# Kernel optimization log

Hardware: AMD Instinct MI355X
Metric: run time of the kernel (lower is better)

## Reference

```python
import jax, jax.numpy as jnp
import numpy as np

D_MODEL = 512
NUM_HEADS = 8
D_K = D_MODEL // NUM_HEADS


def setup_inputs() -> dict:
    key = jax.random.key(0)
    ks = jax.random.split(key, 12)
    B, Sq, Sk = 4, 2048, 2048
    scale = 1.0 / np.sqrt(D_MODEL)
    inp = {
        'query': jax.random.normal(ks[0], (B, Sq, D_MODEL), jnp.float32),
        'key':   jax.random.normal(ks[1], (B, Sk, D_MODEL), jnp.float32),
        'value': jax.random.normal(ks[2], (B, Sk, D_MODEL), jnp.float32),
        'wq': jax.random.normal(ks[3], (D_MODEL, D_MODEL), jnp.float32) * scale,
        'bq': jnp.zeros((D_MODEL,), jnp.float32),
        'wk': jax.random.normal(ks[4], (D_MODEL, D_MODEL), jnp.float32) * scale,
        'bk': jnp.zeros((D_MODEL,), jnp.float32),
        'wv': jax.random.normal(ks[5], (D_MODEL, D_MODEL), jnp.float32) * scale,
        'bv': jnp.zeros((D_MODEL,), jnp.float32),
        'wo': jax.random.normal(ks[6], (D_MODEL, D_MODEL), jnp.float32) * scale,
        'bo': jnp.zeros((D_MODEL,), jnp.float32),
        'ln_g': jnp.ones((D_MODEL,), jnp.float32),
        'ln_b': jnp.zeros((D_MODEL,), jnp.float32),
    }
    return inp


def _layer_norm(x, g, b, eps=1e-5):
    mu = jnp.mean(x, axis=-1, keepdims=True)
    var = jnp.mean(jnp.square(x - mu), axis=-1, keepdims=True)
    return (x - mu) * jax.lax.rsqrt(var + eps) * g + b


def reference(query, key, value, wq, bq, wk, bk, wv, bv, wo, bo, ln_g, ln_b):
    B, Sq, _ = query.shape
    Sk = key.shape[1]
    residual = query
    # projections: torch Linear computes x @ W^T + b; here wq is (out,in)-free:
    # we store weights as (d_model, d_model) and use x @ W + b (equivalent param space)
    Q = (query @ wq + bq).reshape(B, Sq, NUM_HEADS, D_K).transpose(0, 2, 1, 3)
    K = (key   @ wk + bk).reshape(B, Sk, NUM_HEADS, D_K).transpose(0, 2, 1, 3)
    V = (value @ wv + bv).reshape(B, Sk, NUM_HEADS, D_K).transpose(0, 2, 1, 3)
    scores = jnp.einsum('bhqd,bhkd->bhqk', Q, K) / jnp.sqrt(jnp.float32(D_K))
    attn = jax.nn.softmax(scores, axis=-1)  # dropout is identity in eval
    context = jnp.einsum('bhqk,bhkd->bhqd', attn, V)
    context = context.transpose(0, 2, 1, 3).reshape(B, Sq, D_MODEL)
    out = context @ wo + bo
    return _layer_norm(out + residual, ln_g, ln_b)
```

## Files before the change

### kernel.cpp

```cpp
#include <hip/hip_runtime.h>
#include <cstdint>
#include <cstddef>

typedef unsigned short u16;
typedef __bf16 bf16x8 __attribute__((ext_vector_type(8)));
typedef __bf16 bf16x4 __attribute__((ext_vector_type(4)));
typedef float f32x4 __attribute__((ext_vector_type(4)));

#define DEVI __device__ __forceinline__

DEVI u16 f2bf(float f){
  union { float f; unsigned u; } v; v.f = f;
  unsigned r = v.u + 0x7fffu + ((v.u >> 16) & 1u);
  return (u16)(r >> 16);
}

#if defined(__has_builtin)
#if __has_builtin(__builtin_amdgcn_exp2f)
#define EXP2F(x) __builtin_amdgcn_exp2f(x)
#else
#define EXP2F(x) exp2f(x)
#endif
#else
#define EXP2F(x) exp2f(x)
#endif

#define MFMA16(a,b,c) __builtin_amdgcn_mfma_f32_16x16x32_bf16((a),(b),(c),0,0,0)

DEVI void gload_lds16(const void* g, void* l){
  __builtin_amdgcn_global_load_lds(
      (const __attribute__((address_space(1))) void*)g,
      (__attribute__((address_space(3))) void*)l, 16, 0, 0);
}

#define PIPE_SYNC do{ asm volatile("s_waitcnt vmcnt(0)" ::: "memory"); \
    __builtin_amdgcn_s_barrier(); \
    __builtin_amdgcn_sched_barrier(0); }while(0)


__global__ void k_prep_x(const float* __restrict__ q, const float* __restrict__ k,
                         const float* __restrict__ v, u16* __restrict__ xb){
  size_t t = (size_t)blockIdx.x*blockDim.x + threadIdx.x;
  size_t base = t*8;
  const float* s;
  if (base < 4194304u)      s = q + base;
  else if (base < 8388608u) s = k + (base - 4194304u);
  else                      s = v + (base - 8388608u);
  float4 a = *(const float4*)s;
  float4 b = *(const float4*)(s+4);
  ushort4 o0, o1;
  o0.x=f2bf(a.x); o0.y=f2bf(a.y); o0.z=f2bf(a.z); o0.w=f2bf(a.w);
  o1.x=f2bf(b.x); o1.y=f2bf(b.y); o1.z=f2bf(b.z); o1.w=f2bf(b.w);
  *(ushort4*)(xb + base)     = o0;
  *(ushort4*)(xb + base + 4) = o1;
}

__global__ void k_prep_w(const float* __restrict__ w0, const float* __restrict__ w1,
                         const float* __restrict__ w2, const float* __restrict__ w3,
                         u16* __restrict__ wt){
  __shared__ u16 tile[64][72];
  int p = blockIdx.z;
  const float* W = (p==0)?w0:((p==1)?w1:((p==2)?w2:w3));
  int k0 = blockIdx.x*64, n0 = blockIdx.y*64;
  int t = threadIdx.x;
  int tr = t >> 4, tc = t & 15;
  #pragma unroll
  for (int pass=0; pass<4; pass++){
    int row = pass*16 + tr;
    float4 a = *(const float4*)(W + (size_t)(k0+row)*512 + n0 + tc*4);
    tile[row][tc*4+0] = f2bf(a.x);
    tile[row][tc*4+1] = f2bf(a.y);
    tile[row][tc*4+2] = f2bf(a.z);
    tile[row][tc*4+3] = f2bf(a.w);
  }
  __syncthreads();
  #pragma unroll
  for (int pass=0; pass<4; pass++){
    int n = pass*16 + tr;
    ushort4 o;
    o.x = tile[tc*4+0][n];
    o.y = tile[tc*4+1][n];
    o.z = tile[tc*4+2][n];
    o.w = tile[tc*4+3][n];
    *(ushort4*)(wt + (size_t)p*262144 + (size_t)(n0+n)*512 + k0 + tc*4) = o;
  }
}

__global__ __launch_bounds__(256)
void k_gemm_qkv(const u16* __restrict__ xb, const u16* __restrict__ wt,
                const float* __restrict__ bq, const float* __restrict__ bk,
                const float* __restrict__ bv,
                u16* __restrict__ qb, u16* __restrict__ kb, u16* __restrict__ vt){
  int l = threadIdx.x & 63, w = threadIdx.x >> 6;
  int lr = l & 15, lg = l >> 4;
  int f = blockIdx.x;
  int xcd = f & 7, j0 = f >> 3;
  int pm   = xcd*24 + (j0 >> 2);
  int nblk = j0 & 3;
  int p    = pm >> 6, mblk = pm & 63;
  int wr = w >> 1, wc = w & 1;

  const float* bias = (p==0)?bq:((p==1)?bk:bv);
  float osc = (p==0)? (0.125f*1.44269504088896340736f) : 1.0f;

  const char* Ag = (const char*)(xb + (size_t)p*4194304 + (size_t)mblk*128*512);
  const char* Bg = (const char*)(wt + (size_t)p*262144  + (size_t)nblk*128*512);

  __shared__ __align__(16) u16 Albuf[2][8192];
  __shared__ __align__(16) u16 Blbuf[2][8192];

  int r8 = l >> 3, sl = l & 7;

  #define STAGE_G(t, buf) do{ \
    _Pragma("unroll") \
    for (int cc=0; cc<4; ++cc){ \
      int c = w*4 + cc; int row = c*8 + r8; \
      int sw = (sl ^ (row & 7)) << 4; \
      gload_lds16(Ag + (size_t)row*1024 + (size_t)(t)*128 + sw, (char*)Albuf[buf] + c*1024); \
      gload_lds16(Bg + (size_t)row*1024 + (size_t)(t)*128 + sw, (char*)Blbuf[buf] + c*1024); \
    } }while(0)

  STAGE_G(0, 0);
  PIPE_SYNC;

  f32x4 acc[4][4] = {};
  for (int t = 0; t < 8; ++t){
    int cur = t & 1;
    if (t < 7) STAGE_G(t+1, cur^1);
    const char* Ac = (const char*)Albuf[cur];
    const char* Bc = (const char*)Blbuf[cur];
    #pragma unroll
    for (int kk=0;kk<2;kk++){
      int ks = ((kk*4 + lg) ^ (lr & 7)) << 4;
      bf16x8 af[4], bfr[4];
      #pragma unroll
      for (int i=0;i<4;i++)
        af[i]  = *(const bf16x8*)(Ac + (wr*64 + i*16 + lr)*128 + ks);
      #pragma unroll
      for (int j=0;j<4;j++)
        bfr[j] = *(const bf16x8*)(Bc + (wc*64 + j*16 + lr)*128 + ks);
      #pragma unroll
      for (int i=0;i<4;i++)
        #pragma unroll
        for (int j=0;j<4;j++)
          acc[i][j] = MFMA16(af[i], bfr[j], acc[i][j]);
    }
    if (t < 7) PIPE_SYNC;
  }
  #undef STAGE_G

  int m0 = mblk*128 + wr*64;
  int n0 = nblk*128 + wc*64;
  if (p < 2){
    u16* outp = (p==0)?qb:kb;
    #pragma unroll
    for (int i=0;i<4;i++){
      #pragma unroll
      for (int j=0;j<4;j++){
        int n = n0 + j*16 + lr;
        int h = n >> 6, d = n & 63;
        float bb = bias[n];
        #pragma unroll
        for (int rg=0;rg<4;rg++){
          int m = m0 + i*16 + 4*lg + rg;
          int b = m >> 11, s = m & 2047;
          float val = (acc[i][j][rg] + bb)*osc;
          __bf16 hb = (__bf16)val;
          outp[(((size_t)b*8 + h)*2048 + s)*64 + d] = *(u16*)&hb;
        }
      }
    }
  } else {
    #pragma unroll
    for (int i=0;i<4;i++){
      #pragma unroll
      for (int j=0;j<4;j++){
        int n = n0 + j*16 + lr;
        int h = n >> 6, d = n & 63;
        float bb = bias[n];
        int m = m0 + i*16 + 4*lg;
        int b = m >> 11, s = m & 2047;
        ushort4 o;
        #pragma unroll
        for (int rg=0;rg<4;rg++){
          __bf16 hb = (__bf16)(acc[i][j][rg] + bb);
          ((u16*)&o)[rg] = *(u16*)&hb;
        }
        *(ushort4*)(vt + (((size_t)(b*8+h)*64 + d)*2048 + s)) = o;
      }
    }
  }
}

__global__ __launch_bounds__(512, 4)
void k_attn(const u16* __restrict__ qbuf, const u16* __restrict__ kbuf,
            const u16* __restrict__ vtb, u16* __restrict__ opart,
            float* __restrict__ lpart){
  int l = threadIdx.x & 63, w = threadIdx.x >> 6;
  int lr = l & 15, lg = l >> 4;
  int f = blockIdx.x;
  int bh    = (f & 7)*4 + ((f >> 3) & 3);
  int rest  = f >> 5;
  int split = rest & 1;
  int q0    = (rest >> 1)*256 + w*32;
  int b = bh >> 3, h = bh & 7;
  int kvbase = split*1024;

  const u16* Qp = qbuf + ((size_t)bh*2048 + q0)*64;
  const char* Kg = (const char*)(kbuf + (size_t)bh*2048*64) + (size_t)kvbase*128;
  const char* Vg = (const char*)(vtb  + (size_t)bh*64*2048) + (size_t)kvbase*2;

  __shared__ __align__(16) u16 Klds[2][4096];
  __shared__ __align__(16) u16 Vlds[2][4096];
  __shared__ __align__(16) u16 Plds[8][2048];
  u16* Pw = Plds[w];

  int r8 = l >> 3, sl = l & 7;

  bf16x8 qf[2][2];
  #pragma unroll
  for (int j=0;j<2;j++)
    #pragma unroll
    for (int kk=0;kk<2;kk++)
      qf[j][kk] = *(const bf16x8*)(Qp + (size_t)(j*16+lr)*64 + kk*32 + lg*8);

  {
    int row = w*8 + r8;
    int sw = (sl ^ (row & 7)) << 4;
    gload_lds16(Kg + (size_t)row*128 + sw,  (char*)Klds[0] + w*1024);
    gload_lds16(Vg + (size_t)row*4096 + sw, (char*)Vlds[0] + w*1024);
  }
  PIPE_SYNC;

  f32x4 oacc[2][4] = {};
  float lsum[2] = {0.f, 0.f};
  const float M = 16.0f;

  for (int t = 0; t < 16; ++t){
    int cur = t & 1;
    if (t < 15){
      int row = w*8 + r8;
      int sw = (sl ^ (row & 7)) << 4;
      gload_lds16(Kg + (size_t)(t+1)*8192 + (size_t)row*128 + sw,
                  (char*)Klds[cur^1] + w*1024);
      gload_lds16(Vg + (size_t)(t+1)*128 + (size_t)row*4096 + sw,
                  (char*)Vlds[cur^1] + w*1024);
    }
    const char* Kc = (const char*)Klds[cur];
    const char* Vc = (const char*)Vlds[cur];
    f32x4 sacc[4][2] = {};
    #pragma unroll
    for (int kk=0;kk<2;kk++){
      bf16x8 kf[4];
      #pragma unroll
      for (int i=0;i<4;i++)
        kf[i] = *(const bf16x8*)(Kc + (i*16+lr)*128 + (((4*kk+lg)^(lr&7))<<4));
      #pragma unroll
      for (int i=0;i<4;i++)
        #pragma unroll
        for (int j=0;j<2;j++)
          sacc[i][j] = MFMA16(kf[i], qf[j][kk], sacc[i][j]);
    }
    #pragma unroll
    for (int j=0;j<2;j++){
      int qrow = lr + 16*j;
      #pragma unroll
      for (int i=0;i<4;i++){
        bf16x4 pk;
        #pragma unroll
        for (int rg=0;rg<4;rg++){
          float pv = EXP2F(sacc[i][j][rg] - M);
          lsum[j] += pv;
          pk[rg] = (__bf16)pv;
        }
        int o    = 8*lg + 32*i;
        int slot = (o >> 4) ^ (qrow & 7);
        *(bf16x4*)((char*)Pw + qrow*128 + (slot<<4) + (o & 15)) = pk;
      }
    }
    #pragma unroll
    for (int kk=0;kk<2;kk++){
      bf16x8 pf[2];
      #pragma unroll
      for (int fi=0;fi<2;fi++){
        int qrow = fi*16 + lr;
        int slot = (4*kk + lg) ^ (qrow & 7);
        pf[fi] = *(const bf16x8*)((char*)Pw + qrow*128 + (slot<<4));
      }
      bf16x8 vf[4];
      #pragma unroll
      for (int fj=0;fj<4;fj++)
        vf[fj] = *(const bf16x8*)(Vc + (fj*16+lr)*128 + (((4*kk+lg)^(lr&7))<<4));
      #pragma unroll
      for (int fi=0;fi<2;fi++)
        #pragma unroll
        for (int fj=0;fj<4;fj++)
          oacc[fi][fj] = MFMA16(pf[fi], vf[fj], oacc[fi][fj]);
    }
    if (t < 15) PIPE_SYNC;
  }

  #pragma unroll
  for (int j=0;j<2;j++){
    lsum[j] += __shfl_xor(lsum[j], 16);
    lsum[j] += __shfl_xor(lsum[j], 32);
  }
  if (lg == 0){
    #pragma unroll
    for (int j=0;j<2;j++)
      lpart[((size_t)split*32 + bh)*2048 + q0 + 16*j + lr] = lsum[j];
  }
  u16* op = opart + (size_t)split*8192*512;
  #pragma unroll
  for (int fi=0;fi<2;fi++){
    #pragma unroll
    for (int fj=0;fj<4;fj++){
      int col = h*64 + fj*16 + lr;
      #pragma unroll
      for (int rg=0;rg<4;rg++){
        int qg = q0 + fi*16 + 4*lg + rg;
        __bf16 hb = (__bf16)oacc[fi][fj][rg];
        op[((size_t)(b*2048 + qg))*512 + col] = *(u16*)&hb;
      }
    }
  }
}

__global__ void k_combine(const u16* __restrict__ opart,
                          const float* __restrict__ lpart,
                          u16* __restrict__ ctx){
  int t = blockIdx.x*256 + threadIdx.x;
  int m  = t >> 6;
  int c8 = (t & 63) * 8;
  int b = m >> 11, q = m & 2047;
  int h = c8 >> 6;
  int bh = b*8 + h;
  float l0 = lpart[(size_t)bh*2048 + q];
  float l1 = lpart[(size_t)(32 + bh)*2048 + q];
  float inv = 1.f / (l0 + l1);
  bf16x8 a0 = *(const bf16x8*)(opart + (size_t)m*512 + c8);
  bf16x8 a1 = *(const bf16x8*)(opart + (size_t)(8192 + m)*512 + c8);
  bf16x8 r;
  #pragma unroll
  for (int e=0;e<8;e++)
    r[e] = (__bf16)(((float)a0[e] + (float)a1[e]) * inv);
  *(bf16x8*)(ctx + (size_t)m*512 + c8) = r;
}

__global__ __launch_bounds__(256)
void k_gemm_o(const u16* __restrict__ ctx, const u16* __restrict__ wto,
              u16* __restrict__ gout){
  int l = threadIdx.x & 63, w = threadIdx.x >> 6;
  int lr = l & 15, lg = l >> 4;
  int f = blockIdx.x;
  int xcd = f & 7, j0 = f >> 3;
  int mblk = xcd*16 + (j0 >> 2);
  int nblk = j0 & 3;
  int wr = w & 1, wc = w >> 1;

  const char* Ag = (const char*)(ctx + (size_t)mblk*64*512);
  const char* Bg = (const char*)(wto + (size_t)nblk*128*512);

  __shared__ __align__(16) u16 Albuf[2][4096];
  __shared__ __align__(16) u16 Blbuf[2][8192];

  int r8 = l >> 3, sl = l & 7;

  #define STAGE_O(t, buf) do{ \
    _Pragma("unroll") \
    for (int cc=0; cc<2; ++cc){ \
      int c = w*2 + cc; int row = c*8 + r8; \
      int sw = (sl ^ (row & 7)) << 4; \
      gload_lds16(Ag + (size_t)row*1024 + (size_t)(t)*128 + sw, (char*)Albuf[buf] + c*1024); \
    } \
    _Pragma("unroll") \
    for (int cc=0; cc<4; ++cc){ \
      int c = w*4 + cc; int row = c*8 + r8; \
      int sw = (sl ^ (row & 7)) << 4; \
      gload_lds16(Bg + (size_t)row*1024 + (size_t)(t)*128 + sw, (char*)Blbuf[buf] + c*1024); \
    } }while(0)

  STAGE_O(0, 0);
  PIPE_SYNC;

  f32x4 acc[2][4] = {};
  for (int t = 0; t < 8; ++t){
    int cur = t & 1;
    if (t < 7) STAGE_O(t+1, cur^1);
    const char* Ac = (const char*)Albuf[cur];
    const char* Bc = (const char*)Blbuf[cur];
    #pragma unroll
    for (int kk=0;kk<2;kk++){
      int ks = ((kk*4 + lg) ^ (lr & 7)) << 4;
      bf16x8 af[2], bfr[4];
      #pragma unroll
      for (int i=0;i<2;i++)
        af[i]  = *(const bf16x8*)(Ac + (wr*32 + i*16 + lr)*128 + ks);
      #pragma unroll
      for (int j=0;j<4;j++)
        bfr[j] = *(const bf16x8*)(Bc + (wc*64 + j*16 + lr)*128 + ks);
      #pragma unroll
      for (int i=0;i<2;i++)
        #pragma unroll
        for (int j=0;j<4;j++)
          acc[i][j] = MFMA16(af[i], bfr[j], acc[i][j]);
    }
    if (t < 7) PIPE_SYNC;
  }
  #undef STAGE_O

  int m0 = mblk*64 + wr*32;
  int n0 = nblk*128 + wc*64;
  #pragma unroll
  for (int i=0;i<2;i++){
    #pragma unroll
    for (int j=0;j<4;j++){
      int n = n0 + j*16 + lr;
      #pragma unroll
      for (int rg=0;rg<4;rg++){
        int m = m0 + i*16 + 4*lg + rg;
        __bf16 hb = (__bf16)acc[i][j][rg];
        gout[(size_t)m*512 + n] = *(u16*)&hb;
      }
    }
  }
}

__global__ __launch_bounds__(256)
void k_ln(const u16* __restrict__ gout, const float* __restrict__ bo,
          const float* __restrict__ resid, const float* __restrict__ g,
          const float* __restrict__ beta, float* __restrict__ out){
  int gid  = blockIdx.x*256 + threadIdx.x;
  int row  = gid >> 6;
  int lane = gid & 63;
  int c0 = lane*8;
  bf16x8 a = *(const bf16x8*)(gout + (size_t)row*512 + c0);
  float4 r0 = *(const float4*)(resid + (size_t)row*512 + c0);
  float4 r1 = *(const float4*)(resid + (size_t)row*512 + c0 + 4);
  float4 b0 = *(const float4*)(bo + c0);
  float4 b1 = *(const float4*)(bo + c0 + 4);
  float v[8];
  v[0]=(float)a[0]+b0.x+r0.x; v[1]=(float)a[1]+b0.y+r0.y;
  v[2]=(float)a[2]+b0.z+r0.z; v[3]=(float)a[3]+b0.w+r0.w;
  v[4]=(float)a[4]+b1.x+r1.x; v[5]=(float)a[5]+b1.y+r1.y;
  v[6]=(float)a[6]+b1.z+r1.z; v[7]=(float)a[7]+b1.w+r1.w;
  float s1 = 0.f, s2 = 0.f;
  #pragma unroll
  for (int e=0;e<8;e++){ s1 += v[e]; s2 += v[e]*v[e]; }
  #pragma unroll
  for (int mk=1; mk<64; mk<<=1){
    s1 += __shfl_xor(s1, mk);
    s2 += __shfl_xor(s2, mk);
  }
  float mu   = s1 * (1.f/512.f);
  float var  = s2 * (1.f/512.f) - mu*mu;
  float rstd = rsqrtf(var + 1e-5f);
  float4 g0 = *(const float4*)(g + c0);
  float4 g1 = *(const float4*)(g + c0 + 4);
  float4 e0 = *(const float4*)(beta + c0);
  float4 e1 = *(const float4*)(beta + c0 + 4);
  float4 o0, o1;
  o0.x=(v[0]-mu)*rstd*g0.x+e0.x; o0.y=(v[1]-mu)*rstd*g0.y+e0.y;
  o0.z=(v[2]-mu)*rstd*g0.z+e0.z; o0.w=(v[3]-mu)*rstd*g0.w+e0.w;
  o1.x=(v[4]-mu)*rstd*g1.x+e1.x; o1.y=(v[5]-mu)*rstd*g1.y+e1.y;
  o1.z=(v[6]-mu)*rstd*g1.z+e1.z; o1.w=(v[7]-mu)*rstd*g1.w+e1.w;
  *(float4*)(out + (size_t)row*512 + c0)     = o0;
  *(float4*)(out + (size_t)row*512 + c0 + 4) = o1;
}

extern "C" void kernel_launch(void* const* d_in, const int* in_sizes, int n_in,
                              void* d_out, int out_size, void* d_ws, size_t ws_size,
                              hipStream_t stream){
  const float* q   = (const float*)d_in[0];
  const float* k   = (const float*)d_in[1];
  const float* v   = (const float*)d_in[2];
  const float* wq  = (const float*)d_in[3];
  const float* bq  = (const float*)d_in[4];
  const float* wk  = (const float*)d_in[5];
  const float* bk  = (const float*)d_in[6];
  const float* wv  = (const float*)d_in[7];
  const float* bv  = (const float*)d_in[8];
  const float* wo  = (const float*)d_in[9];
  const float* bo  = (const float*)d_in[10];
  const float* lng = (const float*)d_in[11];
  const float* lnb = (const float*)d_in[12];
  float* out = (float*)d_out;
  char* ws = (char*)d_ws;
  u16*   xb    = (u16*)(ws + 0);
  u16*   opart = (u16*)(ws + 0);
  float* lpart = (float*)(ws + 16777216);
  u16*   wt    = (u16*)(ws + 25165824);
  u16*   qb    = (u16*)(ws + 27262976);
  u16*   kb    = (u16*)(ws + 35651584);
  u16*   vt    = (u16*)(ws + 44040192);
  u16*   ctx   = (u16*)(ws + 52428800);
  u16*   gout  = (u16*)(ws + 60817408);

  k_prep_x<<<6144, 256, 0, stream>>>(q, k, v, xb);
  k_prep_w<<<dim3(8,8,4), 256, 0, stream>>>(wq, wk, wv, wo, wt);
  k_gemm_qkv<<<768, 256, 0, stream>>>(xb, wt, bq, bk, bv, qb, kb, vt);
  k_attn<<<512, 512, 0, stream>>>(qb, kb, vt, opart, lpart);
  k_combine<<<2048, 256, 0, stream>>>(opart, lpart, ctx);
  k_gemm_o<<<512, 256, 0, stream>>>(ctx, wt + 3*262144, gout);
  k_ln<<<2048, 256, 0, stream>>>(gout, bo, q, lng, lnb, out);
}
```

Measured before the change: 106.0 us.

## Fuse split-K attention combine into output projection GEMM A-tile staging

Removes the separate combine kernel and instead has the output-projection GEMM load both attention partial outputs and partial row sums, normalise them in registers, and write the combined bf16 tile into LDS. This avoids one kernel launch and the write and reread of the intermediate context buffer. In exchange the A operand is no longer loaded asynchronously into LDS, so the GEMM must wait on register loads, do the arithmetic and write LDS before each barrier, and each output tile repeats the combine work across the four N blocks. It also wraps the MFMA sections in the attention and GEMM kernels with s_setprio raises.

New measurement: 105.3 us. No clear change (-0.6%).

```diff
diff --git a/kernel.cpp b/kernel.cpp
--- a/kernel.cpp
+++ b/kernel.cpp
@@ -34,6 +34,10 @@
 }
 
 #define PIPE_SYNC do{ asm volatile("s_waitcnt vmcnt(0)" ::: "memory"); \
+    __builtin_amdgcn_s_barrier(); \
+    __builtin_amdgcn_sched_barrier(0); }while(0)
+
+#define PIPE_SYNC_VL do{ asm volatile("s_waitcnt vmcnt(0) lgkmcnt(0)" ::: "memory"); \
     __builtin_amdgcn_s_barrier(); \
     __builtin_amdgcn_sched_barrier(0); }while(0)
 
@@ -255,11 +259,13 @@
       #pragma unroll
       for (int i=0;i<4;i++)
         kf[i] = *(const bf16x8*)(Kc + (i*16+lr)*128 + (((4*kk+lg)^(lr&7))<<4));
+      __builtin_amdgcn_s_setprio(1);
       #pragma unroll
       for (int i=0;i<4;i++)
         #pragma unroll
         for (int j=0;j<2;j++)
           sacc[i][j] = MFMA16(kf[i], qf[j][kk], sacc[i][j]);
+      __builtin_amdgcn_s_setprio(0);
     }
     #pragma unroll
     for (int j=0;j<2;j++){
@@ -291,11 +297,13 @@
       #pragma unroll
       for (int fj=0;fj<4;fj++)
         vf[fj] = *(const bf16x8*)(Vc + (fj*16+lr)*128 + (((4*kk+lg)^(lr&7))<<4));
+      __builtin_amdgcn_s_setprio(1);
       #pragma unroll
       for (int fi=0;fi<2;fi++)
         #pragma unroll
         for (int fj=0;fj<4;fj++)
           oacc[fi][fj] = MFMA16(pf[fi], vf[fj], oacc[fi][fj]);
+      __builtin_amdgcn_s_setprio(0);
     }
     if (t < 15) PIPE_SYNC;
   }
@@ -326,29 +334,9 @@
   }
 }
 
-__global__ void k_combine(const u16* __restrict__ opart,
-                          const float* __restrict__ lpart,
-                          u16* __restrict__ ctx){
-  int t = blockIdx.x*256 + threadIdx.x;
-  int m  = t >> 6;
-  int c8 = (t & 63) * 8;
-  int b = m >> 11, q = m & 2047;
-  int h = c8 >> 6;
-  int bh = b*8 + h;
-  float l0 = lpart[(size_t)bh*2048 + q];
-  float l1 = lpart[(size_t)(32 + bh)*2048 + q];
-  float inv = 1.f / (l0 + l1);
-  bf16x8 a0 = *(const bf16x8*)(opart + (size_t)m*512 + c8);
-  bf16x8 a1 = *(const bf16x8*)(opart + (size_t)(8192 + m)*512 + c8);
-  bf16x8 r;
-  #pragma unroll
-  for (int e=0;e<8;e++)
-    r[e] = (__bf16)(((float)a0[e] + (float)a1[e]) * inv);
-  *(bf16x8*)(ctx + (size_t)m*512 + c8) = r;
-}
-
 __global__ __launch_bounds__(256)
-void k_gemm_o(const u16* __restrict__ ctx, const u16* __restrict__ wto,
+void k_gemm_o(const u16* __restrict__ op0, const u16* __restrict__ op1,
+              const float* __restrict__ lpart, const u16* __restrict__ wto,
               u16* __restrict__ gout){
   int l = threadIdx.x & 63, w = threadIdx.x >> 6;
   int lr = l & 15, lg = l >> 4;
@@ -358,7 +346,11 @@
   int nblk = j0 & 3;
   int wr = w & 1, wc = w >> 1;
 
-  const char* Ag = (const char*)(ctx + (size_t)mblk*64*512);
+  int bb8 = (mblk >> 5) * 8;
+  int qbase = (mblk & 31) * 64;
+
+  const u16* Ag0 = op0 + (size_t)mblk*64*512;
+  const u16* Ag1 = op1 + (size_t)mblk*64*512;
   const char* Bg = (const char*)(wto + (size_t)nblk*128*512);
 
   __shared__ __align__(16) u16 Albuf[2][4096];
@@ -366,27 +358,49 @@
 
   int r8 = l >> 3, sl = l & 7;
 
-  #define STAGE_O(t, buf) do{ \
+  bf16x8 a0v[2], a1v[2]; float l0v[2], l1v[2];
+  #define A_ISSUE(tt) do{ \
     _Pragma("unroll") \
     for (int cc=0; cc<2; ++cc){ \
       int c = w*2 + cc; int row = c*8 + r8; \
-      int sw = (sl ^ (row & 7)) << 4; \
-      gload_lds16(Ag + (size_t)row*1024 + (size_t)(t)*128 + sw, (char*)Albuf[buf] + c*1024); \
-    } \
+      int ssrc = sl ^ (row & 7); \
+      a0v[cc] = *(const bf16x8*)(Ag0 + (size_t)row*512 + (tt)*64 + ssrc*8); \
+      a1v[cc] = *(const bf16x8*)(Ag1 + (size_t)row*512 + (tt)*64 + ssrc*8); \
+      int q = qbase + row; \
+      l0v[cc] = lpart[(size_t)(bb8 + (tt))*2048 + q]; \
+      l1v[cc] = lpart[(size_t)(32 + bb8 + (tt))*2048 + q]; \
+    } }while(0)
+
+  #define A_WRITE(buf) do{ \
+    _Pragma("unroll") \
+    for (int cc=0; cc<2; ++cc){ \
+      int c = w*2 + cc; \
+      float inv = 1.f / (l0v[cc] + l1v[cc]); \
+      bf16x8 r; \
+      _Pragma("unroll") \
+      for (int e=0;e<8;e++) \
+        r[e] = (__bf16)(((float)a0v[cc][e] + (float)a1v[cc][e]) * inv); \
+      *(bf16x8*)((char*)Albuf[buf] + c*1024 + r8*128 + sl*16) = r; \
+    } }while(0)
+
+  #define B_STAGE(tt, buf) do{ \
     _Pragma("unroll") \
     for (int cc=0; cc<4; ++cc){ \
       int c = w*4 + cc; int row = c*8 + r8; \
       int sw = (sl ^ (row & 7)) << 4; \
-      gload_lds16(Bg + (size_t)row*1024 + (size_t)(t)*128 + sw, (char*)Blbuf[buf] + c*1024); \
+      gload_lds16(Bg + (size_t)row*1024 + (size_t)(tt)*128 + sw, (char*)Blbuf[buf] + c*1024); \
     } }while(0)
 
-  STAGE_O(0, 0);
-  PIPE_SYNC;
+  A_ISSUE(0);
+  B_STAGE(0, 0);
+  asm volatile("s_waitcnt vmcnt(0)" ::: "memory");
+  A_WRITE(0);
+  PIPE_SYNC_VL;
 
   f32x4 acc[2][4] = {};
   for (int t = 0; t < 8; ++t){
     int cur = t & 1;
-    if (t < 7) STAGE_O(t+1, cur^1);
+    if (t < 7){ A_ISSUE(t+1); B_STAGE(t+1, cur^1); }
     const char* Ac = (const char*)Albuf[cur];
     const char* Bc = (const char*)Blbuf[cur];
     #pragma unroll
@@ -399,15 +413,23 @@
       #pragma unroll
       for (int j=0;j<4;j++)
         bfr[j] = *(const bf16x8*)(Bc + (wc*64 + j*16 + lr)*128 + ks);
+      __builtin_amdgcn_s_setprio(1);
       #pragma unroll
       for (int i=0;i<2;i++)
         #pragma unroll
         for (int j=0;j<4;j++)
           acc[i][j] = MFMA16(af[i], bfr[j], acc[i][j]);
-    }
-    if (t < 7) PIPE_SYNC;
-  }
-  #undef STAGE_O
+      __builtin_amdgcn_s_setprio(0);
+    }
+    if (t < 7){
+      asm volatile("s_waitcnt vmcnt(0)" ::: "memory");
+      A_WRITE(cur^1);
+      PIPE_SYNC_VL;
+    }
+  }
+  #undef A_ISSUE
+  #undef A_WRITE
+  #undef B_STAGE
 
   int m0 = mblk*64 + wr*32;
   int n0 = nblk*128 + wc*64;
@@ -493,14 +515,13 @@
   u16*   qb    = (u16*)(ws + 27262976);
   u16*   kb    = (u16*)(ws + 35651584);
   u16*   vt    = (u16*)(ws + 44040192);
-  u16*   ctx   = (u16*)(ws + 52428800);
-  u16*   gout  = (u16*)(ws + 60817408);
+  u16*   gout  = (u16*)(ws + 52428800);
 
   k_prep_x<<<6144, 256, 0, stream>>>(q, k, v, xb);
   k_prep_w<<<dim3(8,8,4), 256, 0, stream>>>(wq, wk, wv, wo, wt);
   k_gemm_qkv<<<768, 256, 0, stream>>>(xb, wt, bq, bk, bv, qb, kb, vt);
   k_attn<<<512, 512, 0, stream>>>(qb, kb, vt, opart, lpart);
-  k_combine<<<2048, 256, 0, stream>>>(opart, lpart, ctx);
-  k_gemm_o<<<512, 256, 0, stream>>>(ctx, wt + 3*262144, gout);
+  k_gemm_o<<<512, 256, 0, stream>>>(opart, opart + (size_t)8192*512, lpart,
+                                    wt + 3*262144, gout);
   k_ln<<<2048, 256, 0, stream>>>(gout, bo, q, lng, lnb, out);
 }
```
